# Optimization experiments

Hardware: AMD Instinct MI355X
Metric: run time of the kernel (lower is better)

Reference implementation:

```python
import jax, jax.numpy as jnp
import numpy as np

D_MODEL = 1024
NUM_HEADS = 16
HEAD_DIM = D_MODEL // NUM_HEADS
BATCH, SEQ = 2, 2048


def setup_inputs() -> dict:
    key = jax.random.key(0)
    ks = jax.random.split(key, 5)
    scale = 1.0 / np.sqrt(D_MODEL)  # ~xavier magnitude
    x = jax.random.normal(ks[0], (BATCH, SEQ, D_MODEL), dtype=jnp.float32)
    Wq = jax.random.normal(ks[1], (D_MODEL, D_MODEL), dtype=jnp.float32) * scale
    Wk = jax.random.normal(ks[2], (D_MODEL, D_MODEL), dtype=jnp.float32) * scale
    Wv = jax.random.normal(ks[3], (D_MODEL, D_MODEL), dtype=jnp.float32) * scale
    Wo = jax.random.normal(ks[4], (D_MODEL, D_MODEL), dtype=jnp.float32) * scale
    z = jnp.zeros((D_MODEL,), dtype=jnp.float32)
    return {"x": x, "Wq": Wq, "bq": z, "Wk": Wk, "bk": z, "Wv": Wv, "bv": z, "Wo": Wo, "bo": z}


def reference(x, Wq, bq, Wk, bk, Wv, bv, Wo, bo):
    B, S, _ = x.shape
    H, Dh = NUM_HEADS, HEAD_DIM
    # torch Linear convention: y = x @ W^T + b
    q = (x @ Wq.T + bq).reshape(B, S, H, Dh)
    k = (x @ Wk.T + bk).reshape(B, S, H, Dh)
    v = (x @ Wv.T + bv).reshape(B, S, H, Dh)
    # scores: [B, H, S, S]
    scores = jnp.einsum('bqhd,bkhd->bhqk', q, k) / np.sqrt(Dh).astype(np.float32)
    attn = jax.nn.softmax(scores, axis=-1)
    out = jnp.einsum('bhqk,bkhd->bqhd', attn, v).reshape(B, S, H * Dh)
    return out @ Wo.T + bo
```

## Files before the change

kernel.cpp:

```cpp
#include <hip/hip_runtime.h>
#include <hip/hip_bf16.h>

typedef __bf16 bf16;
typedef __bf16 bf16x8 __attribute__((ext_vector_type(8)));
typedef __bf16 bf16x4 __attribute__((ext_vector_type(4)));
typedef float f32x4 __attribute__((ext_vector_type(4)));
typedef float f32x16 __attribute__((ext_vector_type(16)));
typedef unsigned int u32x4 __attribute__((ext_vector_type(4)));

constexpr int DM = 1024, NH = 16, DH = 64, NB = 2, SQ = 2048;
constexpr int MTOT = NB * SQ;
constexpr float QSCALE = 0.125f * 1.44269504088896f;

__device__ __forceinline__ void gld_lds16(const bf16* g, bf16* l) {
  __builtin_amdgcn_global_load_lds(
      (const __attribute__((address_space(1))) void*)g,
      (__attribute__((address_space(3))) void*)l, 16, 0, 0);
}

__global__ __launch_bounds__(256) void cvt5(
    const float* __restrict__ s0, const float* __restrict__ s1,
    const float* __restrict__ s2, const float* __restrict__ s3,
    const float* __restrict__ s4,
    bf16* __restrict__ d0, bf16* __restrict__ d1, bf16* __restrict__ d2,
    bf16* __restrict__ d3, bf16* __restrict__ d4) {
  const int idx = (blockIdx.x * 256 + threadIdx.x) * 4;
  const float* src; bf16* dst; int off;
  if (idx < 4 * DM * DM) {
    off = idx & (DM * DM - 1);
    switch (idx >> 20) {
      case 0: src = s0; dst = d0; break;
      case 1: src = s1; dst = d1; break;
      case 2: src = s2; dst = d2; break;
      default: src = s3; dst = d3; break;
    }
  } else {
    src = s4; dst = d4; off = idx - 4 * DM * DM;
  }
  const float4 v = *(const float4*)(src + off);
  *(bf16x4*)(dst + off) = (bf16x4){(bf16)v.x, (bf16)v.y, (bf16)v.z, (bf16)v.w};
}

template <int BM, typename OutT>
__device__ __forceinline__ void gemm_tile(
    const bf16* __restrict__ A, const bf16* __restrict__ Bm,
    const float* __restrict__ bias, OutT* __restrict__ C,
    int rowA0, int rowB0, int N, int K, bool bias_row, float cscale,
    bf16* sA, bf16* sB) {
  constexpr int NT = (BM == 128) ? 4 : 2;
  const int tid = threadIdx.x;
  const int wave = tid >> 6, lane = tid & 63;
  const int quad = lane >> 4, l16 = lane & 15;
  const int row0w = (BM == 128) ? (wave >> 1) * 64 : 0;
  const int col0w = (BM == 128) ? (wave & 1) * 64 : wave * 32;

  f32x4 acc[4][NT];
#pragma unroll
  for (int i = 0; i < 4; i++)
#pragma unroll
    for (int j = 0; j < NT; j++) acc[i][j] = (f32x4){0.f, 0.f, 0.f, 0.f};

  const int srow = lane >> 3;
  const int scol = ((lane & 7) ^ srow) * 8;

  for (int kt = 0; kt < K; kt += 64) {
#pragma unroll
    for (int i = 0; i < BM / 32; i++) {
      const int r = i * 32 + wave * 8;
      gld_lds16(A + (size_t)(rowA0 + r + srow) * K + kt + scol, &sA[r * 64]);
    }
#pragma unroll
    for (int i = 0; i < 4; i++) {
      const int r = i * 32 + wave * 8;
      gld_lds16(Bm + (size_t)(rowB0 + r + srow) * K + kt + scol, &sB[r * 64]);
    }
    __syncthreads();
#pragma unroll
    for (int kk = 0; kk < 64; kk += 32) {
      bf16x8 aF[4], bF[NT];
      const int slot = (((kk >> 3) + quad) ^ (l16 & 7)) << 3;
#pragma unroll
      for (int mt = 0; mt < 4; mt++)
        aF[mt] = *(const bf16x8*)&sA[(row0w + mt * 16 + l16) * 64 + slot];
#pragma unroll
      for (int nt = 0; nt < NT; nt++)
        bF[nt] = *(const bf16x8*)&sB[(col0w + nt * 16 + l16) * 64 + slot];
#pragma unroll
      for (int mt = 0; mt < 4; mt++)
#pragma unroll
        for (int nt = 0; nt < NT; nt++)
          acc[mt][nt] = __builtin_amdgcn_mfma_f32_16x16x32_bf16(aF[mt], bF[nt], acc[mt][nt], 0, 0, 0);
    }
    __syncthreads();
  }

#pragma unroll
  for (int mt = 0; mt < 4; mt++) {
#pragma unroll
    for (int nt = 0; nt < NT; nt++) {
#pragma unroll
      for (int r = 0; r < 4; r++) {
        const int row = rowA0 + row0w + mt * 16 + quad * 4 + r;
        const int col = rowB0 + col0w + nt * 16 + l16;
        const float bb = bias_row ? bias[row] : bias[col];
        C[(size_t)row * N + col] = (OutT)((acc[mt][nt][r] + bb) * cscale);
      }
    }
  }
}

__global__ __launch_bounds__(256, 4) void qkv_gemm(
    const bf16* __restrict__ xb, const bf16* __restrict__ Wqb,
    const bf16* __restrict__ Wkb, const bf16* __restrict__ Wvb,
    const float* __restrict__ bq, const float* __restrict__ bk,
    const float* __restrict__ bv,
    bf16* __restrict__ Qw, bf16* __restrict__ Kw, bf16* __restrict__ VTw) {
  __shared__ alignas(16) bf16 sA[128 * 64];
  __shared__ alignas(16) bf16 sB[128 * 64];
  if (blockIdx.z == 0) {
    gemm_tile<128, bf16>(xb, Wqb, bq, Qw, blockIdx.x * 128, blockIdx.y * 128, DM, DM, false, QSCALE, sA, sB);
  } else if (blockIdx.z == 1) {
    gemm_tile<128, bf16>(xb, Wkb, bk, Kw, blockIdx.x * 128, blockIdx.y * 128, DM, DM, false, 1.0f, sA, sB);
  } else {
    const int id = blockIdx.y * 32 + blockIdx.x;
    gemm_tile<128, bf16>(Wvb, xb, bv, VTw, (id >> 5) * 128, (id & 31) * 128, MTOT, DM, true, 1.0f, sA, sB);
  }
}

__global__ __launch_bounds__(256, 4) void out_gemm(
    const bf16* __restrict__ A, const bf16* __restrict__ Bm,
    const float* __restrict__ bias, float* __restrict__ C) {
  __shared__ alignas(16) bf16 sA[64 * 64];
  __shared__ alignas(16) bf16 sB[128 * 64];
  gemm_tile<64, float>(A, Bm, bias, C, blockIdx.x * 64, blockIdx.y * 128, DM, DM, false, 1.0f, sA, sB);
}

__global__ __launch_bounds__(256, 2) void attn(
    const bf16* __restrict__ Q, const bf16* __restrict__ Kq,
    const bf16* __restrict__ VT, bf16* __restrict__ O) {
  __shared__ alignas(16) bf16 sK[2][64 * 64];
  __shared__ alignas(16) bf16 sV[2][64 * 64];
  const int tid = threadIdx.x, wave = tid >> 6, lane = tid & 63;
  const int l32 = lane & 31, half = lane >> 5;
  const int hb = blockIdx.x, qt = blockIdx.y;
  const int h = hb & 15, b = hb >> 4;

  const bf16* Qg = Q + (size_t)(b * SQ + qt * 128 + wave * 32) * DM + h * DH;
  const bf16* Kg = Kq + (size_t)(b * SQ) * DM + h * DH;
  const bf16* Vg = VT + (size_t)(h * DH) * MTOT + b * SQ;

  const int srow = lane >> 3, scol = ((lane & 7) ^ srow) * 8;

  auto stageKV = [&](int t, int buf) {
#pragma unroll
    for (int i = 0; i < 2; i++) {
      const int r = (wave * 2 + i) * 8;
      gld_lds16(Kg + (size_t)(t * 64 + r + srow) * DM + scol, &sK[buf][r * 64]);
      gld_lds16(Vg + (size_t)(r + srow) * MTOT + t * 64 + scol, &sV[buf][r * 64]);
    }
  };

  bf16x8 qF[4];
#pragma unroll
  for (int kk = 0; kk < 4; kk++)
    qF[kk] = *(const bf16x8*)(Qg + (size_t)l32 * DM + kk * 16 + half * 8);

  f32x16 o_acc[2];
#pragma unroll
  for (int nd = 0; nd < 2; nd++)
#pragma unroll
    for (int i = 0; i < 16; i++) o_acc[nd][i] = 0.f;
  float lsum = 0.f;

  stageKV(0, 0);
  for (int t = 0; t < 32; ++t) {
    __syncthreads();
    if (t + 1 < 32) stageKV(t + 1, (t + 1) & 1);
    const bf16* cK = sK[t & 1];
    const bf16* cV = sV[t & 1];
    const int sw7 = l32 & 7;

    f32x16 sacc[2];
#pragma unroll
    for (int nt = 0; nt < 2; nt++)
#pragma unroll
      for (int i = 0; i < 16; i++) sacc[nt][i] = 0.f;

    bf16x8 kf[2][4];
#pragma unroll
    for (int nt = 0; nt < 2; nt++)
#pragma unroll
      for (int kk = 0; kk < 4; kk++)
        kf[nt][kk] = *(const bf16x8*)&cK[(nt * 32 + l32) * 64 + (((kk * 2 + half) ^ sw7) << 3)];
    __builtin_amdgcn_s_setprio(1);
#pragma unroll
    for (int nt = 0; nt < 2; nt++)
#pragma unroll
      for (int kk = 0; kk < 4; kk++)
        sacc[nt] = __builtin_amdgcn_mfma_f32_32x32x16_bf16(kf[nt][kk], qF[kk], sacc[nt], 0, 0, 0);
    __builtin_amdgcn_s_setprio(0);

#pragma unroll
    for (int nt = 0; nt < 2; nt++) {
      float p[16];
#pragma unroll
      for (int i = 0; i < 16; i++) {
        p[i] = __builtin_amdgcn_exp2f(sacc[nt][i]);
        lsum += p[i];
      }
      unsigned int w[8];
#pragma unroll
      for (int i = 0; i < 8; i++)
        asm("v_cvt_pk_bf16_f32 %0, %1, %2" : "=v"(w[i]) : "v"(p[2 * i]), "v"(p[2 * i + 1]));
      asm("v_permlane32_swap_b32 %0, %1" : "+v"(w[0]), "+v"(w[2]));
      asm("v_permlane32_swap_b32 %0, %1" : "+v"(w[1]), "+v"(w[3]));
      asm("v_permlane32_swap_b32 %0, %1" : "+v"(w[4]), "+v"(w[6]));
      asm("v_permlane32_swap_b32 %0, %1" : "+v"(w[5]), "+v"(w[7]));
#pragma unroll
      for (int s = 0; s < 2; s++) {
        const u32x4 pw = (s == 0) ? (u32x4){w[0], w[1], w[2], w[3]}
                                  : (u32x4){w[4], w[5], w[6], w[7]};
        const bf16x8 pb = __builtin_bit_cast(bf16x8, pw);
        const int ks = nt * 2 + s;
        bf16x8 vf[2];
#pragma unroll
        for (int nd = 0; nd < 2; nd++)
          vf[nd] = *(const bf16x8*)&cV[(nd * 32 + l32) * 64 + (((ks * 2 + half) ^ sw7) << 3)];
        __builtin_amdgcn_s_setprio(1);
#pragma unroll
        for (int nd = 0; nd < 2; nd++)
          o_acc[nd] = __builtin_amdgcn_mfma_f32_32x32x16_bf16(vf[nd], pb, o_acc[nd], 0, 0, 0);
        __builtin_amdgcn_s_setprio(0);
      }
    }
  }

  const float lother = __shfl(lsum, lane ^ 32, 64);
  const float inv = 1.0f / (lsum + lother);

  bf16* Op = O + (size_t)(b * SQ + qt * 128 + wave * 32 + l32) * DM + h * DH;
#pragma unroll
  for (int nd = 0; nd < 2; nd++) {
#pragma unroll
    for (int g = 0; g < 4; g++) {
      bf16x4 ov;
#pragma unroll
      for (int r = 0; r < 4; r++) ov[r] = (bf16)(o_acc[nd][g * 4 + r] * inv);
      *(bf16x4*)(Op + nd * 32 + g * 8 + half * 4) = ov;
    }
  }
}

extern "C" void kernel_launch(void* const* d_in, const int* in_sizes, int n_in,
                              void* d_out, int out_size, void* d_ws, size_t ws_size,
                              hipStream_t stream) {
  const float* x  = (const float*)d_in[0];
  const float* Wq = (const float*)d_in[1];
  const float* bq = (const float*)d_in[2];
  const float* Wk = (const float*)d_in[3];
  const float* bk = (const float*)d_in[4];
  const float* Wv = (const float*)d_in[5];
  const float* bv = (const float*)d_in[6];
  const float* Wo = (const float*)d_in[7];
  const float* bo = (const float*)d_in[8];
  float* out = (float*)d_out;

  bf16* ws   = (bf16*)d_ws;
  bf16* xb   = ws;
  bf16* Wqb  = ws + (size_t)MTOT * DM;
  bf16* Wkb  = Wqb + (size_t)DM * DM;
  bf16* Wvb  = Wkb + (size_t)DM * DM;
  bf16* Wob  = Wvb + (size_t)DM * DM;
  bf16* Qw   = Wob + (size_t)DM * DM;
  bf16* Kw   = Qw + (size_t)MTOT * DM;
  bf16* VTw  = Kw + (size_t)MTOT * DM;
  bf16* Cw   = VTw + (size_t)MTOT * DM;

  const dim3 blk(256);
  cvt5<<<dim3((4 * DM * DM + MTOT * DM) / 1024, 1), blk, 0, stream>>>(
      Wq, Wk, Wv, Wo, x, Wqb, Wkb, Wvb, Wob, xb);
  qkv_gemm<<<dim3(32, 8, 3), blk, 0, stream>>>(xb, Wqb, Wkb, Wvb, bq, bk, bv, Qw, Kw, VTw);
  attn<<<dim3(NH * NB, SQ / 128), blk, 0, stream>>>(Qw, Kw, VTw, Cw);
  out_gemm<<<dim3(MTOT / 64, DM / 128), blk, 0, stream>>>(Cw, Wob, bo, out);
}
```

Before: 180.5 us.

## Split attention KV sequence across two wave groups with LDS combine

The attention block grows to 512 threads, and two groups of four waves each process half of the key/value sequence for the same 128 query rows. The partial output accumulators and row sums are combined through LDS at the end. The aim is to double the waves per block and halve the serial loop length, hiding latency better in a grid of only 512 blocks. The cost is twice the LDS, an extra reduction step with two barriers, and possible register-pressure limits under the 512,4 launch bounds. The row-sum accumulation also moves to four partial sums.

```diff
diff --git a/kernel.cpp b/kernel.cpp
--- a/kernel.cpp
+++ b/kernel.cpp
@@ -135,28 +135,29 @@
   gemm_tile<64, float>(A, Bm, bias, C, blockIdx.x * 64, blockIdx.y * 128, DM, DM, false, 1.0f, sA, sB);
 }
 
-__global__ __launch_bounds__(256, 2) void attn(
+__global__ __launch_bounds__(512, 4) void attn(
     const bf16* __restrict__ Q, const bf16* __restrict__ Kq,
     const bf16* __restrict__ VT, bf16* __restrict__ O) {
-  __shared__ alignas(16) bf16 sK[2][64 * 64];
-  __shared__ alignas(16) bf16 sV[2][64 * 64];
+  __shared__ alignas(16) bf16 sK[2][2][64 * 64];
+  __shared__ alignas(16) bf16 sV[2][2][64 * 64];
   const int tid = threadIdx.x, wave = tid >> 6, lane = tid & 63;
+  const int grp = wave >> 2, w4 = wave & 3;
   const int l32 = lane & 31, half = lane >> 5;
   const int hb = blockIdx.x, qt = blockIdx.y;
   const int h = hb & 15, b = hb >> 4;
 
-  const bf16* Qg = Q + (size_t)(b * SQ + qt * 128 + wave * 32) * DM + h * DH;
-  const bf16* Kg = Kq + (size_t)(b * SQ) * DM + h * DH;
-  const bf16* Vg = VT + (size_t)(h * DH) * MTOT + b * SQ;
+  const bf16* Qg = Q + (size_t)(b * SQ + qt * 128 + w4 * 32) * DM + h * DH;
+  const bf16* Kg = Kq + (size_t)(b * SQ + grp * 1024) * DM + h * DH;
+  const bf16* Vg = VT + (size_t)(h * DH) * MTOT + b * SQ + grp * 1024;
 
   const int srow = lane >> 3, scol = ((lane & 7) ^ srow) * 8;
 
   auto stageKV = [&](int t, int buf) {
 #pragma unroll
     for (int i = 0; i < 2; i++) {
-      const int r = (wave * 2 + i) * 8;
-      gld_lds16(Kg + (size_t)(t * 64 + r + srow) * DM + scol, &sK[buf][r * 64]);
-      gld_lds16(Vg + (size_t)(r + srow) * MTOT + t * 64 + scol, &sV[buf][r * 64]);
+      const int r = (w4 * 2 + i) * 8;
+      gld_lds16(Kg + (size_t)(t * 64 + r + srow) * DM + scol, &sK[grp][buf][r * 64]);
+      gld_lds16(Vg + (size_t)(r + srow) * MTOT + t * 64 + scol, &sV[grp][buf][r * 64]);
     }
   };
 
@@ -170,14 +171,14 @@
   for (int nd = 0; nd < 2; nd++)
 #pragma unroll
     for (int i = 0; i < 16; i++) o_acc[nd][i] = 0.f;
-  float lsum = 0.f;
+  f32x4 lsum4 = (f32x4){0.f, 0.f, 0.f, 0.f};
 
   stageKV(0, 0);
-  for (int t = 0; t < 32; ++t) {
+  for (int t = 0; t < 16; ++t) {
     __syncthreads();
-    if (t + 1 < 32) stageKV(t + 1, (t + 1) & 1);
-    const bf16* cK = sK[t & 1];
-    const bf16* cV = sV[t & 1];
+    if (t + 1 < 16) stageKV(t + 1, (t + 1) & 1);
+    const bf16* cK = sK[grp][t & 1];
+    const bf16* cV = sV[grp][t & 1];
     const int sw7 = l32 & 7;
 
     f32x16 sacc[2];
@@ -206,7 +207,7 @@
 #pragma unroll
       for (int i = 0; i < 16; i++) {
         p[i] = __builtin_amdgcn_exp2f(sacc[nt][i]);
-        lsum += p[i];
+        lsum4[i & 3] += p[i];
       }
       unsigned int w[8];
 #pragma unroll
@@ -235,10 +236,38 @@
     }
   }
 
-  const float lother = __shfl(lsum, lane ^ 32, 64);
-  const float inv = 1.0f / (lsum + lother);
-
-  bf16* Op = O + (size_t)(b * SQ + qt * 128 + wave * 32 + l32) * DM + h * DH;
+  const float lsum = (lsum4[0] + lsum4[1]) + (lsum4[2] + lsum4[3]);
+  __syncthreads();
+  float* cbO = (float*)&sK[0][0][0];
+  float* cbL = (float*)&sV[0][0][0];
+  if (grp == 1) {
+    f32x4* dst = (f32x4*)&cbO[(w4 * 64 + lane) * 32];
+#pragma unroll
+    for (int nd = 0; nd < 2; nd++)
+#pragma unroll
+      for (int g = 0; g < 4; g++)
+        dst[nd * 4 + g] = (f32x4){o_acc[nd][g * 4 + 0], o_acc[nd][g * 4 + 1],
+                                  o_acc[nd][g * 4 + 2], o_acc[nd][g * 4 + 3]};
+    cbL[w4 * 64 + lane] = lsum;
+  }
+  __syncthreads();
+  if (grp == 1) return;
+
+  const f32x4* src = (const f32x4*)&cbO[(w4 * 64 + lane) * 32];
+  float lt = lsum + cbL[w4 * 64 + lane];
+#pragma unroll
+  for (int nd = 0; nd < 2; nd++)
+#pragma unroll
+    for (int g = 0; g < 4; g++) {
+      const f32x4 v = src[nd * 4 + g];
+#pragma unroll
+      for (int r = 0; r < 4; r++) o_acc[nd][g * 4 + r] += v[r];
+    }
+
+  const float lother = __shfl(lt, lane ^ 32, 64);
+  const float inv = 1.0f / (lt + lother);
+
+  bf16* Op = O + (size_t)(b * SQ + qt * 128 + w4 * 32 + l32) * DM + h * DH;
 #pragma unroll
   for (int nd = 0; nd < 2; nd++) {
 #pragma unroll
@@ -280,6 +309,6 @@
   cvt5<<<dim3((4 * DM * DM + MTOT * DM) / 1024, 1), blk, 0, stream>>>(
       Wq, Wk, Wv, Wo, x, Wqb, Wkb, Wvb, Wob, xb);
   qkv_gemm<<<dim3(32, 8, 3), blk, 0, stream>>>(xb, Wqb, Wkb, Wvb, bq, bk, bv, Qw, Kw, VTw);
-  attn<<<dim3(NH * NB, SQ / 128), blk, 0, stream>>>(Qw, Kw, VTw, Cw);
+  attn<<<dim3(NH * NB, SQ / 128), dim3(512), 0, stream>>>(Qw, Kw, VTw, Cw);
   out_gemm<<<dim3(MTOT / 64, DM / 128), blk, 0, stream>>>(Cw, Wob, bo, out);
 }
```

Result: no change. 181.7 us (+0.7%).
